# Optimization experiments

Measured on AMD Instinct MI355X. Metric: run time of the kernel, lower is better.

The kernel has to match this reference:

```python
import jax, jax.numpy as jnp
import numpy as np

# Multi-scale AvgPool3d pyramid (stride 1, zero padding, count_include_pad=True as in torch)
KERNELS = [(1, 1, 1), (1, 5, 5), (3, 13, 13), (5, 23, 23), (7, 31, 31), (9, 41, 41)]
WEIGHTS = [w / 100.0 for w in [20, 20, 20, 20, 20, 20, 10, 10]]
EPS = 1e-7  # BatchDiceLoss epsilon


def avgpool3d(x, k):
    # x: [B, C, D, H, W]; separable sum-pool per axis then divide by full kernel size
    # (equivalent to torch AvgPool3d with count_include_pad=True, stride 1, pad=(k-1)//2)
    y = x
    for axis, ks in zip((2, 3, 4), k):
        if ks > 1:
            window = [1] * 5
            window[axis] = ks
            pad = [(0, 0)] * 5
            pad[axis] = (ks // 2, ks // 2)
            y = jax.lax.reduce_window(y, 0.0, jax.lax.add, tuple(window), (1,) * 5, tuple(pad))
    return y / float(np.prod(k))


def batch_dice(pred, target):
    # BatchDiceLoss([1.0]): single label channel 0, flattened over the whole batch
    p = pred[:, 0].reshape(-1)
    t = target[:, 0].reshape(-1)
    inter = jnp.sum(p * t)
    return 1.0 - (2.0 * inter) / (jnp.sum(p) + jnp.sum(t) + EPS)


def multi_scale_dc(pred, target):
    loss = 0.0
    for k in KERNELS:
        pp = avgpool3d(avgpool3d(pred, k), k)   # pool applied twice per scale
        tt = avgpool3d(avgpool3d(target, k), k)
        loss = loss + batch_dice(pp, tt)
    return loss / len(KERNELS)


def setup_inputs() -> dict:
    key = jax.random.key(0)
    ks = jax.random.split(key, 14)
    vol = (4, 1, 28, 160, 160)
    u = lambda k: jax.random.uniform(k, vol, dtype=jnp.float32)
    return {
        "pr_core_c": u(ks[0]),
        "pr_core_p": u(ks[1]),
        "gt_core": u(ks[2]),
        "pr_lesion_c": u(ks[3]),
        "pr_lesion_p": u(ks[4]),
        "gt_lesion": u(ks[5]),
        "pr_penu_c": u(ks[6]),
        "pr_penu_p": u(ks[7]),
        "gt_penu": u(ks[8]),
        "output": jax.random.uniform(ks[9], (4, 6, 28, 160, 160), dtype=jnp.float32),
        "off_core_c": jax.random.normal(ks[10], (4, 3), dtype=jnp.float32),
        "off_penu_p": jax.random.normal(ks[11], (4, 3), dtype=jnp.float32),
        "off_target_c": jax.random.normal(ks[12], (4, 3), dtype=jnp.float32),
        "off_target_p": jax.random.normal(ks[13], (4, 3), dtype=jnp.float32),
    }


def reference(pr_core_c, pr_core_p, gt_core, pr_lesion_c, pr_lesion_p, gt_lesion,
              pr_penu_c, pr_penu_p, gt_penu, output,
              off_core_c, off_penu_p, off_target_c, off_target_p):
    loss = WEIGHTS[0] * multi_scale_dc(pr_core_c, gt_core)
    loss += WEIGHTS[1] * multi_scale_dc(pr_core_p, gt_core)
    loss += WEIGHTS[2] * multi_scale_dc(pr_lesion_c, gt_lesion)
    loss += WEIGHTS[3] * multi_scale_dc(pr_lesion_p, gt_lesion)
    loss += WEIGHTS[4] * multi_scale_dc(pr_penu_c, gt_penu)
    loss += WEIGHTS[5] * multi_scale_dc(pr_penu_p, gt_penu)
    # temporal monotonicity penalty: mean(|diff| - diff) per consecutive time pair
    diff = output[:, 1:] - output[:, :-1]           # [B, T-1, D, H, W]
    loss += WEIGHTS[6] * jnp.sum(jnp.mean(jnp.abs(diff) - diff, axis=(0, 2, 3, 4)))
    loss += WEIGHTS[7] * jnp.mean(jnp.abs(off_core_c - off_target_c))
    loss += WEIGHTS[7] * jnp.mean(jnp.abs(off_penu_p - off_target_p))
    return loss
```

## Files before the change

kernel.cpp:

```cpp
#include <hip/hip_runtime.h>


#define DIMB 4
#define DIMD 28
#define DIMH 160
#define DIMW 160
#define HW   (DIMH * DIMW)
#define DHW  (DIMD * HW)
#define VOL_N (DIMB * DHW)
#define PGRID 640
#define NSLOTS 91
#define DICE_EPS 1e-7
#define TBL_OFF (480 * 1024)

__device__ __forceinline__ float u2f(int pos, int k, int L) {
    if (k == 1) return 1.f;
    int r = k >> 1;
    float s = 0.f;
    for (int j = max(pos - r, 0); j <= min(pos + r, L - 1); ++j)
        s += (float)(min(j + r, L - 1) - max(j - r, 0) + 1);
    return s / (float)(k * k);
}

__device__ __forceinline__ float wave_sum(float v) {
#pragma unroll
    for (int o = 1; o < 64; o <<= 1) v += __shfl_xor(v, o, 64);
    return v;
}

template<int K>
__device__ __forceinline__ void box4_col(float (&x)[28]) {
    constexpr int R = K / 2;
    constexpr float INVK = 1.f / (float)K;
#pragma unroll
    for (int p = 0; p < 4; ++p) {
        float y[28];
        float s = 0.f;
#pragma unroll
        for (int j = 0; j <= R; ++j) s += x[j];
        y[0] = s;
#pragma unroll
        for (int i = 1; i < 28; ++i) {
            if (i + R < 28) s += x[i + R];
            if (i - R - 1 >= 0) s -= x[i - R - 1];
            y[i] = s;
        }
#pragma unroll
        for (int i = 0; i < 28; ++i) x[i] = y[i] * INVK;
    }
}

template<int K>
__device__ __forceinline__ void hstore(const float (&raw)[40],
                                       unsigned char* __restrict__ ob,
                                       int l, int c, int wl, int h0)
{
    constexpr int R = K / 2;
    constexpr float INVK = 1.f / (float)K;
    float ox[40];
#pragma unroll
    for (int i = 0; i < 40; ++i) ox[i] = raw[i];
#pragma unroll
    for (int pass = 0; pass < 4; ++pass) {
        float lo[R], hi[R];
#pragma unroll
        for (int i = 0; i < R; ++i) {
            float a = __shfl(ox[40 - R + i], l - 16, 64);
            lo[i] = (c == 0) ? 0.f : a;
            float b = __shfl(ox[i], l + 16, 64);
            hi[i] = (c == 3) ? 0.f : b;
        }
#define HWIN(j) ((j) < R ? lo[(j)] : ((j) < R + 40 ? ox[(j) - R] : hi[(j) - R - 40]))
        float out[40];
        float s = 0.f;
#pragma unroll
        for (int j = 0; j <= 2 * R; ++j) s += HWIN(j);
        out[0] = s * INVK;
#pragma unroll
        for (int i = 1; i < 40; ++i) {
            s += HWIN(i + 2 * R) - HWIN(i - 1);
            out[i] = s * INVK;
        }
#undef HWIN
#pragma unroll
        for (int i = 0; i < 40; ++i) ox[i] = out[i];
    }
#pragma unroll
    for (int i = 0; i < 40; ++i)
        ob[(h0 + i) * DIMW + wl] = (unsigned char)__float2uint_rn(ox[i] * 255.f);
}

__global__ __launch_bounds__(256) void hpool_tbl(const float* __restrict__ g0,
    const float* __restrict__ g1, const float* __restrict__ g2,
    unsigned char* __restrict__ bufs, float* __restrict__ tbl)
{
    int bx = blockIdx.x;
    if (bx < 840) {
        int u = bx * 2 + (threadIdx.x >> 7);
        int tt = threadIdx.x & 127;
        int g = u / 560, r = u - g * 560;
        int bd = r / 5, wt = r - bd * 5;
        const float* in = (g == 0) ? g0 : (g == 1) ? g1 : g2;
        int l = tt & 63, v = tt >> 6;
        int c = l >> 4, wl = v * 16 + (l & 15), h0 = c * 40;
        const float* base = in + (size_t)bd * HW + wt * 32;
        float raw[40];
#pragma unroll
        for (int i = 0; i < 40; ++i) raw[i] = base[(h0 + i) * DIMW + wl];
        unsigned char* ob = bufs + (size_t)g * 5 * VOL_N + (size_t)bd * HW + wt * 32;
        hstore<5> (raw, ob + 0 * (size_t)VOL_N, l, c, wl, h0);
        hstore<13>(raw, ob + 1 * (size_t)VOL_N, l, c, wl, h0);
        hstore<23>(raw, ob + 2 * (size_t)VOL_N, l, c, wl, h0);
        hstore<31>(raw, ob + 3 * (size_t)VOL_N, l, c, wl, h0);
        hstore<41>(raw, ob + 4 * (size_t)VOL_N, l, c, wl, h0);
    } else {
        const int KDa[6] = {1, 1, 3, 5, 7, 9};
        const int KHa[6] = {1, 5, 13, 23, 31, 41};
        for (int e = threadIdx.x; e < 1128; e += 256) {
            if (e < 960) tbl[e] = u2f(e % 160, KHa[e / 160], DIMH);
            else {
                int q = e - 960;
                tbl[e] = u2f(q % 28, KDa[q / 28], DIMD);
            }
        }
    }
}

template<int K>
__device__ __forceinline__ void wpool_to_S(const unsigned char* __restrict__ tb,
    float (*S)[164], int t, int l, int rr, int c, bool act)
{
    constexpr int R = K / 2;
    const float INV = 1.0f / (255.0f * (float)K * (float)K * (float)K * (float)K);
    float ox[20];
#pragma unroll
    for (int i = 0; i < 20; ++i) ox[i] = 0.f;
    if (act) {
        unsigned int u[5];
#pragma unroll
        for (int q = 0; q < 5; ++q) u[q] = *(const unsigned int*)(tb + 4 * q);
#pragma unroll
        for (int q = 0; q < 5; ++q) {
#pragma unroll
            for (int j = 0; j < 4; ++j)
                ox[4 * q + j] = (float)((u[q] >> (8 * j)) & 0xFFu);
        }
    }
#pragma unroll
    for (int pass = 0; pass < 4; ++pass) {
        float lo[R], hi[R];
#pragma unroll
        for (int i = 0; i < R; ++i) {
            float a = __shfl(ox[20 - R + i], l - 1, 64);
            lo[i] = (c == 0) ? 0.f : a;
            float b = __shfl(ox[i], l + 1, 64);
            hi[i] = (c == 7) ? 0.f : b;
        }
#define WWIN(j) ((j) < R ? lo[(j)] : ((j) < R + 20 ? ox[(j) - R] : hi[(j) - R - 20]))
        float out[20];
        float s = 0.f;
#pragma unroll
        for (int j = 0; j <= 2 * R; ++j) s += WWIN(j);
        out[0] = s;
#pragma unroll
        for (int i = 1; i < 20; ++i) {
            s += WWIN(i + 2 * R) - WWIN(i - 1);
            out[i] = s;
        }
#undef WWIN
#pragma unroll
        for (int i = 0; i < 20; ++i) ox[i] = out[i];
    }
    if (act) {
#pragma unroll
        for (int i = 0; i < 20; ++i) S[rr][c * 20 + i] = ox[i] * INV;
    }
    __syncthreads();
}

template<int K, int KD>
__device__ __forceinline__ void wd_scale(const unsigned char* __restrict__ tb,
    const float4* __restrict__ c4, const float4* __restrict__ p4, int base4,
    float (*S)[164], float* red2, int t, int l, int wid, int rr, int c, bool act,
    double* __restrict__ partials, int slot_c, int slot_p, int bh)
{
    wpool_to_S<K>(tb, S, t, l, rr, c, act);
    if constexpr (KD > 1) {
        if (t < DIMW) {
            float col[28];
#pragma unroll
            for (int j = 0; j < 28; ++j) col[j] = S[j][t];
            box4_col<KD>(col);
#pragma unroll
            for (int j = 0; j < 28; ++j) S[j][t] = col[j];
        }
        __syncthreads();
    }
    float aic = 0.f, aip = 0.f;
    for (int e4 = t; e4 < 1120; e4 += 256) {
        int dd = e4 / 40, w4 = e4 - dd * 40;
        int fi = base4 + dd * (HW / 4) + w4;
        float4 vc = c4[fi], vp = p4[fi];
        const float4 sv = *(const float4*)&S[dd][4 * w4];
        aic += vc.x * sv.x + vc.y * sv.y + vc.z * sv.z + vc.w * sv.w;
        aip += vp.x * sv.x + vp.y * sv.y + vp.z * sv.z + vp.w * sv.w;
    }
    float r1 = wave_sum(aic), r2 = wave_sum(aip);
    if (l == 0) { red2[wid * 2] = r1; red2[wid * 2 + 1] = r2; }
    __syncthreads();
    if (t < 2) {
        double rv = (double)red2[t] + red2[2 + t] + red2[4 + t] + red2[6 + t];
        partials[(size_t)(t == 0 ? slot_c : slot_p) * PGRID + bh] = rv;
    }
}

__global__ __launch_bounds__(256) void wd_mix(const unsigned char* __restrict__ bufs,
    const float* __restrict__ pc0, const float* __restrict__ pp0,
    const float* __restrict__ pc1, const float* __restrict__ pp1,
    const float* __restrict__ pc2, const float* __restrict__ pp2,
    const float* __restrict__ tr0, const float* __restrict__ tr1,
    const float* __restrict__ tr2, const float* __restrict__ o6,
    const float* __restrict__ tbl, double* __restrict__ partials)
{
    __shared__ __align__(16) float S[DIMD][164];
    __shared__ float redS[4][24];
    int bx0 = blockIdx.x;
    int t = threadIdx.x;

    if (bx0 < 9600) {
        int w = (bx0 & 7) * 1200 + (bx0 >> 3);
        int u = w / 5, q = w - u * 5;
        int g = u / PGRID, bh = u - g * PGRID;
        int b = bh / DIMH, h = bh - b * DIMH;
        const float* pc = (g == 0) ? pc0 : (g == 1) ? pc1 : pc2;
        const float* pp = (g == 0) ? pp0 : (g == 1) ? pp1 : pp2;
        size_t base0 = (size_t)b * DHW + (size_t)h * DIMW;
        int base4 = b * (DHW / 4) + h * 40;
        const float4* c4 = (const float4*)pc;
        const float4* p4 = (const float4*)pp;
        int l = t & 63, wid = t >> 6;
        int rr = wid * 7 + (l >> 3), c = l & 7;
        bool act = (l < 56);
        int sbuf = 4 - q;
        const unsigned char* tb = bufs + (size_t)(g * 5 + sbuf) * VOL_N
                                + base0 + (size_t)rr * HW + c * 20;
        int s = 5 - q;
        int slot_c = (2 * g) * 6 + s, slot_p = (2 * g + 1) * 6 + s;
        switch (q) {
            case 0: wd_scale<41, 9>(tb, c4, p4, base4, S, &redS[0][0], t, l, wid, rr, c, act, partials, slot_c, slot_p, bh); break;
            case 1: wd_scale<31, 7>(tb, c4, p4, base4, S, &redS[0][0], t, l, wid, rr, c, act, partials, slot_c, slot_p, bh); break;
            case 2: wd_scale<23, 5>(tb, c4, p4, base4, S, &redS[0][0], t, l, wid, rr, c, act, partials, slot_c, slot_p, bh); break;
            case 3: wd_scale<13, 3>(tb, c4, p4, base4, S, &redS[0][0], t, l, wid, rr, c, act, partials, slot_c, slot_p, bh); break;
            default: wd_scale<5, 1>(tb, c4, p4, base4, S, &redS[0][0], t, l, wid, rr, c, act, partials, slot_c, slot_p, bh); break;
        }
        return;
    }

    if (bx0 < 11520) {
        int db = bx0 - 9600;
        int g = db / PGRID, blk = db - g * PGRID;
        const float* pc = (g == 0) ? pc0 : (g == 1) ? pc1 : pc2;
        const float* pp = (g == 0) ? pp0 : (g == 1) ? pp1 : pp2;
        const float* tr = (g == 0) ? tr0 : (g == 1) ? tr1 : tr2;
        const float4* c4p = (const float4*)pc;
        const float4* p4p = (const float4*)pp;
        const float4* t4p = (const float4*)tr;
        float vals[20];
#pragma unroll
        for (int i = 0; i < 20; ++i) vals[i] = 0.f;
        const int N4 = VOL_N / 4;
        for (int i4 = blk * 256 + t; i4 < N4; i4 += PGRID * 256) {
            int w4 = i4 % 40;
            int rest = i4 / 40;
            int h = rest % DIMH;
            int d = (rest / DIMH) % DIMD;
            float4 vc = c4p[i4], vp = p4p[i4], vt = t4p[i4];
            vals[0] += vc.x*vt.x + vc.y*vt.y + vc.z*vt.z + vc.w*vt.w;
            vals[1] += vp.x*vt.x + vp.y*vt.y + vp.z*vt.z + vp.w*vt.w;
#pragma unroll
            for (int s = 0; s < 6; ++s) {
                float cdh = tbl[960 + s * 28 + d] * tbl[s * 160 + h];
                const float4 cw = *(const float4*)(tbl + s * 160 + 4 * w4);
                vals[2 + s]  += cdh * (cw.x*vc.x + cw.y*vc.y + cw.z*vc.z + cw.w*vc.w);
                vals[8 + s]  += cdh * (cw.x*vp.x + cw.y*vp.y + cw.z*vp.z + cw.w*vp.w);
                vals[14 + s] += cdh * (cw.x*vt.x + cw.y*vt.y + cw.z*vt.z + cw.w*vt.w);
            }
        }
        int lane = t & 63, wid = t >> 6;
#pragma unroll
        for (int i = 0; i < 20; ++i) {
            float rv = wave_sum(vals[i]);
            if (lane == 0) redS[wid][i] = rv;
        }
        __syncthreads();
        if (t < 20) {
            double rv = (double)redS[0][t] + redS[1][t] + redS[2][t] + redS[3][t];
            int slot;
            if (t == 0) slot = (2 * g) * 6;
            else if (t == 1) slot = (2 * g + 1) * 6;
            else {
                int i = t - 2, vv = i / 6, s = i % 6;
                slot = (vv == 0) ? 36 + (2 * g) * 6 + s
                     : (vv == 1) ? 36 + (2 * g + 1) * 6 + s
                                 : 72 + g * 6 + s;
            }
            partials[(size_t)slot * PGRID + blk] = rv;
        }
        return;
    }

    int mb = bx0 - 11520;
    const int N4 = VOL_N / 4, PB = N4 / DIMB;
    float acc = 0.f;
    const float4* p = (const float4*)o6;
    for (int i = mb * 256 + t; i < N4; i += PGRID * 256) {
        int b = i / PB, r4 = i - b * PB;
        size_t a = (size_t)(b * 6) * PB + r4;
        float4 prev = p[a];
#pragma unroll
        for (int cc = 1; cc < 6; ++cc) {
            float4 cur = p[a + (size_t)cc * PB];
            acc += fmaxf(prev.x - cur.x, 0.f) + fmaxf(prev.y - cur.y, 0.f)
                 + fmaxf(prev.z - cur.z, 0.f) + fmaxf(prev.w - cur.w, 0.f);
            prev = cur;
        }
    }
    float rv = wave_sum(acc * 2.f);
    int lane = t & 63, wid = t >> 6;
    if (lane == 0) redS[wid][0] = rv;
    __syncthreads();
    if (t == 0)
        partials[(size_t)90 * PGRID + mb] =
            (double)redS[0][0] + redS[1][0] + redS[2][0] + redS[3][0];
}

__global__ __launch_bounds__(64) void fin_pre(const double* __restrict__ partials,
                                              double* __restrict__ ssum)
{
    int slot = blockIdx.x, t = threadIdx.x;
    double a = 0.0;
    for (int i = t; i < PGRID; i += 64) a += partials[(size_t)slot * PGRID + i];
#pragma unroll
    for (int o = 1; o < 64; o <<= 1) a += __shfl_xor(a, o, 64);
    if (t == 0) ssum[slot] = a;
}

__global__ void finalize(const double* __restrict__ ssum,
                         const float* __restrict__ off_a,
                         const float* __restrict__ off_b,
                         const float* __restrict__ off_ta,
                         const float* __restrict__ off_tb,
                         float* __restrict__ out)
{
    if (threadIdx.x == 0) {
        double loss = 0.0;
        for (int pair = 0; pair < 6; ++pair) {
            for (int s = 0; s < 6; ++s) {
                double inter = ssum[pair * 6 + s];
                double sp = ssum[36 + pair * 6 + s];
                double st = ssum[72 + (pair / 2) * 6 + s];
                loss += 0.2 * (1.0 - 2.0 * inter / (sp + st + DICE_EPS)) / 6.0;
            }
        }
        loss += 0.1 * (ssum[90] / (double)VOL_N);
        double oa = 0.0, ob = 0.0;
        for (int i = 0; i < 12; ++i) {
            oa += fabs((double)off_a[i] - (double)off_ta[i]);
            ob += fabs((double)off_b[i] - (double)off_tb[i]);
        }
        loss += 0.1 * (oa / 12.0) + 0.1 * (ob / 12.0);
        out[0] = (float)loss;
    }
}

extern "C" void kernel_launch(void* const* d_in, const int* in_sizes, int n_in,
                              void* d_out, int out_size, void* d_ws, size_t ws_size,
                              hipStream_t stream)
{
    double* partials = (double*)d_ws;
    double* ssum = partials + (size_t)NSLOTS * PGRID;
    float* tbl = (float*)((char*)d_ws + TBL_OFF);
    unsigned char* bufs = (unsigned char*)d_ws + 512 * 1024;

    const float* pred[6] = {(const float*)d_in[0], (const float*)d_in[1],
                            (const float*)d_in[3], (const float*)d_in[4],
                            (const float*)d_in[6], (const float*)d_in[7]};
    const float* gt[3] = {(const float*)d_in[2], (const float*)d_in[5],
                          (const float*)d_in[8]};

    hpool_tbl<<<841, 256, 0, stream>>>(gt[0], gt[1], gt[2], bufs, tbl);
    wd_mix<<<12160, 256, 0, stream>>>(bufs, pred[0], pred[1], pred[2], pred[3],
                                      pred[4], pred[5], gt[0], gt[1], gt[2],
                                      (const float*)d_in[9], tbl, partials);
    fin_pre<<<NSLOTS, 64, 0, stream>>>(partials, ssum);
    finalize<<<1, 64, 0, stream>>>(ssum,
                                   (const float*)d_in[10], (const float*)d_in[11],
                                   (const float*)d_in[12], (const float*)d_in[13],
                                   (float*)d_out);
}
```

Baseline: 133.3 us.

## Pack two H rows into half2 for W and D box pooling

Result: faster. 114.5 us (-14.1%).

```diff
diff --git a/kernel.cpp b/kernel.cpp
--- a/kernel.cpp
+++ b/kernel.cpp
@@ -1,4 +1,5 @@
 #include <hip/hip_runtime.h>
+#include <hip/hip_fp16.h>
 
 
 #define DIMB 4
@@ -28,26 +29,9 @@
     return v;
 }
 
-template<int K>
-__device__ __forceinline__ void box4_col(float (&x)[28]) {
-    constexpr int R = K / 2;
-    constexpr float INVK = 1.f / (float)K;
-#pragma unroll
-    for (int p = 0; p < 4; ++p) {
-        float y[28];
-        float s = 0.f;
-#pragma unroll
-        for (int j = 0; j <= R; ++j) s += x[j];
-        y[0] = s;
-#pragma unroll
-        for (int i = 1; i < 28; ++i) {
-            if (i + R < 28) s += x[i + R];
-            if (i - R - 1 >= 0) s -= x[i - R - 1];
-            y[i] = s;
-        }
-#pragma unroll
-        for (int i = 0; i < 28; ++i) x[i] = y[i] * INVK;
-    }
+__device__ __forceinline__ __half2 shfl_h2(__half2 v, int src) {
+    int x = __shfl(*reinterpret_cast<int*>(&v), src, 64);
+    return *reinterpret_cast<__half2*>(&x);
 }
 
 template<int K>
@@ -126,46 +110,57 @@
     }
 }
 
-template<int K>
-__device__ __forceinline__ void wpool_to_S(const unsigned char* __restrict__ tb,
-    float (*S)[164], int t, int l, int rr, int c, bool act)
+template<int K, int KD>
+__device__ __forceinline__ void wd_scale_pk(const unsigned char* __restrict__ tbA,
+    const float4* __restrict__ c4, const float4* __restrict__ p4, int base4,
+    unsigned int (*S)[164], float (*redS)[4], int t, int l, int wid, int rr,
+    int c, bool act, double* __restrict__ partials, int slot_c, int slot_p,
+    int bhA)
 {
     constexpr int R = K / 2;
-    const float INV = 1.0f / (255.0f * (float)K * (float)K * (float)K * (float)K);
-    float ox[20];
-#pragma unroll
-    for (int i = 0; i < 20; ++i) ox[i] = 0.f;
+    const __half2 INVK2 = __float2half2_rn(1.f / (float)K);
+    const __half2 Z2 = __float2half2_rn(0.f);
+    __half2 ox[20];
     if (act) {
-        unsigned int u[5];
-#pragma unroll
-        for (int q = 0; q < 5; ++q) u[q] = *(const unsigned int*)(tb + 4 * q);
+        unsigned int uA[5], uB[5];
 #pragma unroll
         for (int q = 0; q < 5; ++q) {
-#pragma unroll
-            for (int j = 0; j < 4; ++j)
-                ox[4 * q + j] = (float)((u[q] >> (8 * j)) & 0xFFu);
-        }
+            uA[q] = *(const unsigned int*)(tbA + 4 * q);
+            uB[q] = *(const unsigned int*)(tbA + DIMW + 4 * q);
+        }
+#pragma unroll
+        for (int q = 0; q < 5; ++q) {
+#pragma unroll
+            for (int j = 0; j < 4; ++j) {
+                float fA = (float)((uA[q] >> (8 * j)) & 0xFFu);
+                float fB = (float)((uB[q] >> (8 * j)) & 0xFFu);
+                ox[4 * q + j] = __floats2half2_rn(fA, fB);
+            }
+        }
+    } else {
+#pragma unroll
+        for (int i = 0; i < 20; ++i) ox[i] = Z2;
     }
 #pragma unroll
     for (int pass = 0; pass < 4; ++pass) {
-        float lo[R], hi[R];
+        __half2 lo[R], hi[R];
 #pragma unroll
         for (int i = 0; i < R; ++i) {
-            float a = __shfl(ox[20 - R + i], l - 1, 64);
-            lo[i] = (c == 0) ? 0.f : a;
-            float b = __shfl(ox[i], l + 1, 64);
-            hi[i] = (c == 7) ? 0.f : b;
+            __half2 a = shfl_h2(ox[20 - R + i], l - 1);
+            lo[i] = (c == 0) ? Z2 : a;
+            __half2 b = shfl_h2(ox[i], l + 1);
+            hi[i] = (c == 7) ? Z2 : b;
         }
 #define WWIN(j) ((j) < R ? lo[(j)] : ((j) < R + 20 ? ox[(j) - R] : hi[(j) - R - 20]))
-        float out[20];
-        float s = 0.f;
-#pragma unroll
-        for (int j = 0; j <= 2 * R; ++j) s += WWIN(j);
-        out[0] = s;
+        __half2 out[20];
+        __half2 s = Z2;
+#pragma unroll
+        for (int j = 0; j <= 2 * R; ++j) s = __hadd2(s, WWIN(j));
+        out[0] = __hmul2(s, INVK2);
 #pragma unroll
         for (int i = 1; i < 20; ++i) {
-            s += WWIN(i + 2 * R) - WWIN(i - 1);
-            out[i] = s;
+            s = __hadd2(s, __hsub2(WWIN(i + 2 * R), WWIN(i - 1)));
+            out[i] = __hmul2(s, INVK2);
         }
 #undef WWIN
 #pragma unroll
@@ -173,44 +168,69 @@
     }
     if (act) {
 #pragma unroll
-        for (int i = 0; i < 20; ++i) S[rr][c * 20 + i] = ox[i] * INV;
+        for (int i = 0; i < 20; ++i)
+            S[rr][c * 20 + i] = *reinterpret_cast<unsigned int*>(&ox[i]);
     }
     __syncthreads();
-}
-
-template<int K, int KD>
-__device__ __forceinline__ void wd_scale(const unsigned char* __restrict__ tb,
-    const float4* __restrict__ c4, const float4* __restrict__ p4, int base4,
-    float (*S)[164], float* red2, int t, int l, int wid, int rr, int c, bool act,
-    double* __restrict__ partials, int slot_c, int slot_p, int bh)
-{
-    wpool_to_S<K>(tb, S, t, l, rr, c, act);
     if constexpr (KD > 1) {
+        constexpr int RD = KD / 2;
+        const __half2 INVKD2 = __float2half2_rn(1.f / (float)KD);
         if (t < DIMW) {
-            float col[28];
-#pragma unroll
-            for (int j = 0; j < 28; ++j) col[j] = S[j][t];
-            box4_col<KD>(col);
-#pragma unroll
-            for (int j = 0; j < 28; ++j) S[j][t] = col[j];
+            __half2 x[28];
+#pragma unroll
+            for (int j = 0; j < 28; ++j)
+                x[j] = *reinterpret_cast<const __half2*>(&S[j][t]);
+#pragma unroll
+            for (int p = 0; p < 4; ++p) {
+                __half2 y[28];
+                __half2 s = Z2;
+#pragma unroll
+                for (int j = 0; j <= RD; ++j) s = __hadd2(s, x[j]);
+                y[0] = s;
+#pragma unroll
+                for (int i = 1; i < 28; ++i) {
+                    if (i + RD < 28) s = __hadd2(s, x[i + RD]);
+                    if (i - RD - 1 >= 0) s = __hsub2(s, x[i - RD - 1]);
+                    y[i] = s;
+                }
+#pragma unroll
+                for (int i = 0; i < 28; ++i) x[i] = __hmul2(y[i], INVKD2);
+            }
+#pragma unroll
+            for (int j = 0; j < 28; ++j)
+                S[j][t] = *reinterpret_cast<unsigned int*>(&x[j]);
         }
         __syncthreads();
     }
-    float aic = 0.f, aip = 0.f;
+    float aicA = 0.f, aipA = 0.f, aicB = 0.f, aipB = 0.f;
     for (int e4 = t; e4 < 1120; e4 += 256) {
         int dd = e4 / 40, w4 = e4 - dd * 40;
         int fi = base4 + dd * (HW / 4) + w4;
-        float4 vc = c4[fi], vp = p4[fi];
-        const float4 sv = *(const float4*)&S[dd][4 * w4];
-        aic += vc.x * sv.x + vc.y * sv.y + vc.z * sv.z + vc.w * sv.w;
-        aip += vp.x * sv.x + vp.y * sv.y + vp.z * sv.z + vp.w * sv.w;
-    }
-    float r1 = wave_sum(aic), r2 = wave_sum(aip);
-    if (l == 0) { red2[wid * 2] = r1; red2[wid * 2 + 1] = r2; }
+        float4 vcA = c4[fi],      vpA = p4[fi];
+        float4 vcB = c4[fi + 40], vpB = p4[fi + 40];
+        const uint4 sv = *(const uint4*)&S[dd][4 * w4];
+        float2 s0 = __half22float2(*reinterpret_cast<const __half2*>(&sv.x));
+        float2 s1 = __half22float2(*reinterpret_cast<const __half2*>(&sv.y));
+        float2 s2 = __half22float2(*reinterpret_cast<const __half2*>(&sv.z));
+        float2 s3 = __half22float2(*reinterpret_cast<const __half2*>(&sv.w));
+        aicA += vcA.x*s0.x + vcA.y*s1.x + vcA.z*s2.x + vcA.w*s3.x;
+        aipA += vpA.x*s0.x + vpA.y*s1.x + vpA.z*s2.x + vpA.w*s3.x;
+        aicB += vcB.x*s0.y + vcB.y*s1.y + vcB.z*s2.y + vcB.w*s3.y;
+        aipB += vpB.x*s0.y + vpB.y*s1.y + vpB.z*s2.y + vpB.w*s3.y;
+    }
+    const float SC = 1.f / 255.f;
+    float v0 = wave_sum(aicA) * SC, v1 = wave_sum(aipA) * SC;
+    float v2 = wave_sum(aicB) * SC, v3 = wave_sum(aipB) * SC;
+    if (l == 0) {
+        redS[wid][0] = v0; redS[wid][1] = v1;
+        redS[wid][2] = v2; redS[wid][3] = v3;
+    }
     __syncthreads();
-    if (t < 2) {
-        double rv = (double)red2[t] + red2[2 + t] + red2[4 + t] + red2[6 + t];
-        partials[(size_t)(t == 0 ? slot_c : slot_p) * PGRID + bh] = rv;
+    if (t < 4) {
+        double rv = (double)redS[0][t] + redS[1][t] + redS[2][t] + redS[3][t];
+        int slot = (t & 1) ? slot_p : slot_c;
+        int bh = bhA + (t >> 1);
+        partials[(size_t)slot * PGRID + bh] = rv;
     }
 }
 
@@ -222,16 +242,17 @@
     const float* __restrict__ tr2, const float* __restrict__ o6,
     const float* __restrict__ tbl, double* __restrict__ partials)
 {
-    __shared__ __align__(16) float S[DIMD][164];
+    __shared__ __align__(16) unsigned int S[DIMD][164];
     __shared__ float redS[4][24];
     int bx0 = blockIdx.x;
     int t = threadIdx.x;
 
-    if (bx0 < 9600) {
-        int w = (bx0 & 7) * 1200 + (bx0 >> 3);
+    if (bx0 < 4800) {
+        int w = (bx0 & 7) * 600 + (bx0 >> 3);
         int u = w / 5, q = w - u * 5;
-        int g = u / PGRID, bh = u - g * PGRID;
-        int b = bh / DIMH, h = bh - b * DIMH;
+        int g = u / 320, pj = u - g * 320;
+        int bhA = 2 * pj;
+        int b = bhA / DIMH, h = bhA - b * DIMH;
         const float* pc = (g == 0) ? pc0 : (g == 1) ? pc1 : pc2;
         const float* pp = (g == 0) ? pp0 : (g == 1) ? pp1 : pp2;
         size_t base0 = (size_t)b * DHW + (size_t)h * DIMW;
@@ -242,22 +263,22 @@
         int rr = wid * 7 + (l >> 3), c = l & 7;
         bool act = (l < 56);
         int sbuf = 4 - q;
-        const unsigned char* tb = bufs + (size_t)(g * 5 + sbuf) * VOL_N
-                                + base0 + (size_t)rr * HW + c * 20;
+        const unsigned char* tbA = bufs + (size_t)(g * 5 + sbuf) * VOL_N
+                                 + base0 + (size_t)rr * HW + c * 20;
         int s = 5 - q;
         int slot_c = (2 * g) * 6 + s, slot_p = (2 * g + 1) * 6 + s;
         switch (q) {
-            case 0: wd_scale<41, 9>(tb, c4, p4, base4, S, &redS[0][0], t, l, wid, rr, c, act, partials, slot_c, slot_p, bh); break;
-            case 1: wd_scale<31, 7>(tb, c4, p4, base4, S, &redS[0][0], t, l, wid, rr, c, act, partials, slot_c, slot_p, bh); break;
-            case 2: wd_scale<23, 5>(tb, c4, p4, base4, S, &redS[0][0], t, l, wid, rr, c, act, partials, slot_c, slot_p, bh); break;
-            case 3: wd_scale<13, 3>(tb, c4, p4, base4, S, &redS[0][0], t, l, wid, rr, c, act, partials, slot_c, slot_p, bh); break;
-            default: wd_scale<5, 1>(tb, c4, p4, base4, S, &redS[0][0], t, l, wid, rr, c, act, partials, slot_c, slot_p, bh); break;
+            case 0: wd_scale_pk<41, 9>(tbA, c4, p4, base4, S, (float(*)[4])&redS[0][0], t, l, wid, rr, c, act, partials, slot_c, slot_p, bhA); break;
+            case 1: wd_scale_pk<31, 7>(tbA, c4, p4, base4, S, (float(*)[4])&redS[0][0], t, l, wid, rr, c, act, partials, slot_c, slot_p, bhA); break;
+            case 2: wd_scale_pk<23, 5>(tbA, c4, p4, base4, S, (float(*)[4])&redS[0][0], t, l, wid, rr, c, act, partials, slot_c, slot_p, bhA); break;
+            case 3: wd_scale_pk<13, 3>(tbA, c4, p4, base4, S, (float(*)[4])&redS[0][0], t, l, wid, rr, c, act, partials, slot_c, slot_p, bhA); break;
+            default: wd_scale_pk<5, 1>(tbA, c4, p4, base4, S, (float(*)[4])&redS[0][0], t, l, wid, rr, c, act, partials, slot_c, slot_p, bhA); break;
         }
         return;
     }
 
-    if (bx0 < 11520) {
-        int db = bx0 - 9600;
+    if (bx0 < 6720) {
+        int db = bx0 - 4800;
         int g = db / PGRID, blk = db - g * PGRID;
         const float* pc = (g == 0) ? pc0 : (g == 1) ? pc1 : pc2;
         const float* pp = (g == 0) ? pp0 : (g == 1) ? pp1 : pp2;
@@ -309,7 +330,7 @@
         return;
     }
 
-    int mb = bx0 - 11520;
+    int mb = bx0 - 6720;
     const int N4 = VOL_N / 4, PB = N4 / DIMB;
     float acc = 0.f;
     const float4* p = (const float4*)o6;
@@ -389,9 +410,9 @@
                           (const float*)d_in[8]};
 
     hpool_tbl<<<841, 256, 0, stream>>>(gt[0], gt[1], gt[2], bufs, tbl);
-    wd_mix<<<12160, 256, 0, stream>>>(bufs, pred[0], pred[1], pred[2], pred[3],
-                                      pred[4], pred[5], gt[0], gt[1], gt[2],
-                                      (const float*)d_in[9], tbl, partials);
+    wd_mix<<<7360, 256, 0, stream>>>(bufs, pred[0], pred[1], pred[2], pred[3],
+                                     pred[4], pred[5], gt[0], gt[1], gt[2],
+                                     (const float*)d_in[9], tbl, partials);
     fin_pre<<<NSLOTS, 64, 0, stream>>>(partials, ssum);
     finalize<<<1, 64, 0, stream>>>(ssum,
                                    (const float*)d_in[10], (const float*)d_in[11],
```
